# Kernel optimization log

Measured on AMD Instinct MI355X. Metric: run time of the kernel, lower is better.

Reference implementation:

```python
import jax, jax.numpy as jnp
import numpy as np

MARGIN = 0.3
EPS = 1e-12

def setup_inputs() -> dict:
    key = jax.random.key(0)
    k1, k2 = jax.random.split(key)
    n, d, num_classes = 8192, 512, 512
    inputs = jax.random.normal(k1, (n, d), dtype=jnp.float32)
    targets = jax.random.randint(k2, (n,), 0, num_classes, dtype=jnp.int64)
    return {"inputs": inputs, "targets": targets}

def reference(inputs, targets):
    n = inputs.shape[0]
    # pairwise Euclidean distances: ||xi||^2 + ||xj||^2 - 2 xi.xj, clamped & sqrt'd
    sq = jnp.sum(inputs * inputs, axis=1)  # [n]
    dist2 = sq[:, None] + sq[None, :] - 2.0 * (inputs @ inputs.T)
    dist = jnp.sqrt(jnp.clip(dist2, EPS, None))  # [n, n]
    mask = targets[:, None] == targets[None, :]  # [n, n] same-identity mask
    neg_inf = jnp.asarray(-jnp.inf, dist.dtype)
    pos_inf = jnp.asarray(jnp.inf, dist.dtype)
    dist_ap = jnp.max(jnp.where(mask, dist, neg_inf), axis=1)   # hardest positive per row
    dist_an = jnp.min(jnp.where(mask, pos_inf, dist), axis=1)   # hardest negative per row
    # MarginRankingLoss with y=1, mean reduction: mean(relu(dist_ap - dist_an + margin))
    loss = jnp.mean(jnp.maximum(dist_ap - dist_an + MARGIN, 0.0))
    return loss
```

## Files before the change

kernel.cpp:

```cpp
#include <hip/hip_runtime.h>

#define N 8192
#define D 512
#define NSB 32
#define NFULL 1024
#define NQ 64
#define NBRICKS (NFULL + NQ)
#define MARGIN 0.3f

typedef __attribute__((ext_vector_type(4))) int int4v;
typedef __attribute__((ext_vector_type(8))) int int8v;
typedef __attribute__((ext_vector_type(4))) float f32x4;

__device__ __forceinline__ void gload_lds16(const void* g, void* l) {
    __builtin_amdgcn_global_load_lds(
        (const __attribute__((address_space(1))) void*)g,
        (__attribute__((address_space(3))) void*)l,
        16, 0, 0);
}

__device__ __forceinline__ int8v load_frag8(const unsigned char* base, int row, int q) {
    const int v = (2 * q) ^ (row & 7);
    int4v lo = *(const int4v*)(base + row * 128 + v * 16);
    int4v hi = *(const int4v*)(base + row * 128 + (v ^ 1) * 16);
    return __builtin_shufflevector(lo, hi, 0, 1, 2, 3, 4, 5, 6, 7);
}

__global__ void prep_kernel(const float* __restrict__ x,
                            unsigned char* __restrict__ x8,
                            float* __restrict__ sq,
                            unsigned int* __restrict__ apU,
                            unsigned int* __restrict__ anU,
                            int* __restrict__ cnt) {
    if (blockIdx.x == 0 && threadIdx.x == 0) cnt[0] = 0;
    int w = threadIdx.x >> 6, lane = threadIdx.x & 63;
    int row = blockIdx.x * 4 + w;
    const float4* p = (const float4*)(x + (size_t)row * D) + lane * 2;
    float4 v0 = p[0], v1 = p[1];
    float s = v0.x * v0.x + v0.y * v0.y + v0.z * v0.z + v0.w * v0.w
            + v1.x * v1.x + v1.y * v1.y + v1.z * v1.z + v1.w * v1.w;
    int w0 = __builtin_amdgcn_cvt_pk_fp8_f32(v0.x, v0.y, 0, false);
    w0     = __builtin_amdgcn_cvt_pk_fp8_f32(v0.z, v0.w, w0, true);
    int w1 = __builtin_amdgcn_cvt_pk_fp8_f32(v1.x, v1.y, 0, false);
    w1     = __builtin_amdgcn_cvt_pk_fp8_f32(v1.z, v1.w, w1, true);
    ((int2*)(x8 + (size_t)row * D))[lane] = make_int2(w0, w1);
    #pragma unroll
    for (int o = 32; o > 0; o >>= 1) s += __shfl_xor(s, o);
    if (lane == 0) {
        sq[row] = s;
        apU[row] = 0u;
        anU[row] = 0x7f800000u;
    }
}

template <int TN>
__device__ __forceinline__ void brick_body(
    int rowBase, int colBase,
    const unsigned char* __restrict__ xb, const float* __restrict__ sq,
    const int* __restrict__ tgt,
    unsigned int* __restrict__ apU, unsigned int* __restrict__ anU,
    char* smem_raw, float* sqI, float* sqJ, int* tI, int* tJ) {
    constexpr int NC = TN * 32;
    unsigned char* Asm = (unsigned char*)smem_raw;
    unsigned char* Bsm = Asm + 128 * 128;
    float* redAp = (float*)smem_raw;
    float* redAn = redAp + 128 * 34;
    float* colAp = (float*)smem_raw;
    float* colAn = colAp + NC * 10;

    const int tid = threadIdx.x;
    const int w = tid >> 6, lane = tid & 63, q = lane >> 4, c = lane & 15;
    const int wm = w & 1, wn = w >> 1;

    if (tid < 128) { sqI[tid] = sq[rowBase + tid]; tI[tid] = tgt[rowBase + tid]; }
    if (tid < NC)  { sqJ[tid] = sq[colBase + tid]; tJ[tid] = tgt[colBase + tid]; }

    const unsigned char* Ag = xb + (size_t)rowBase * D;
    const unsigned char* Bg = xb + (size_t)colBase * D;

    f32x4 acc[4][TN] = {};

    for (int k0 = 0; k0 < D; k0 += 128) {
        #pragma unroll
        for (int s = 0; s < 4; s++) {
            int p = s * 256 + tid;
            int r = p >> 3, kc = (p & 7) ^ (r & 7);
            gload_lds16(Ag + (size_t)r * D + k0 + kc * 16, Asm + p * 16);
        }
        #pragma unroll
        for (int s = 0; s < TN; s++) {
            int p = s * 256 + tid;
            int r = p >> 3, kc = (p & 7) ^ (r & 7);
            gload_lds16(Bg + (size_t)r * D + k0 + kc * 16, Bsm + p * 16);
        }
        __syncthreads();
        int8v af[4];
        #pragma unroll
        for (int t = 0; t < 4; t++)
            af[t] = load_frag8(Asm, wm * 64 + t * 16 + c, q);
        constexpr int TB = (TN < 4) ? TN : 4;
        #pragma unroll
        for (int tb = 0; tb < TN; tb += TB) {
            int8v bfr[TB];
            #pragma unroll
            for (int t = 0; t < TB; t++)
                bfr[t] = load_frag8(Bsm, wn * (TN * 16) + (tb + t) * 16 + c, q);
            #pragma unroll
            for (int tm = 0; tm < 4; tm++)
                #pragma unroll
                for (int t = 0; t < TB; t++)
                    acc[tm][tb + t] = __builtin_amdgcn_mfma_scale_f32_16x16x128_f8f6f4(
                        af[tm], bfr[t], acc[tm][tb + t],
                        0, 0,
                        0, 0x7F7F7F7Fu, 0, 0x7F7F7F7Fu);
        }
        __syncthreads();
    }

    float sjc[TN]; int tjx[TN];
    #pragma unroll
    for (int tn = 0; tn < TN; tn++) {
        int col_l = wn * (TN * 16) + tn * 16 + c;
        sjc[tn] = sqJ[col_l]; tjx[tn] = tJ[col_l];
    }
    float apc[TN], anc[TN];
    #pragma unroll
    for (int tn = 0; tn < TN; tn++) { apc[tn] = -1e30f; anc[tn] = 1e30f; }
    #pragma unroll
    for (int tm = 0; tm < 4; tm++) {
        #pragma unroll
        for (int r = 0; r < 4; r++) {
            int row_l = wm * 64 + tm * 16 + q * 4 + r;
            float si = sqI[row_l]; int ti = tI[row_l];
            float rp = -1e30f, rn = 1e30f;
            #pragma unroll
            for (int tn = 0; tn < TN; tn++) {
                float p = acc[tm][tn][r];
                bool same = (ti == tjx[tn]);
                float rk = fmaf(-2.0f, p, sjc[tn]);
                float ck = fmaf(-2.0f, p, si);
                rp = fmaxf(rp, same ? rk : -1e30f);
                rn = fminf(rn, same ? 1e30f : rk);
                apc[tn] = fmaxf(apc[tn], same ? ck : -1e30f);
                anc[tn] = fminf(anc[tn], same ? 1e30f : ck);
            }
            redAp[row_l * 34 + wn * 16 + c] = rp;
            redAn[row_l * 34 + wn * 16 + c] = rn;
        }
    }
    __syncthreads();
    if (tid < 128) {
        float ap = -1e30f, an = 1e30f;
        #pragma unroll 8
        for (int u = 0; u < 32; u++) {
            ap = fmaxf(ap, redAp[tid * 34 + u]);
            an = fminf(an, redAn[tid * 34 + u]);
        }
        float apd = fmaxf(sqI[tid] + ap, 0.0f);
        float and_ = fmaxf(sqI[tid] + an, 0.0f);
        atomicMax(&apU[rowBase + tid], __float_as_uint(apd));
        atomicMin(&anU[rowBase + tid], __float_as_uint(and_));
    }
    __syncthreads();
    #pragma unroll
    for (int tn = 0; tn < TN; tn++) {
        int col_l = wn * (TN * 16) + tn * 16 + c;
        colAp[col_l * 10 + wm * 4 + q] = apc[tn];
        colAn[col_l * 10 + wm * 4 + q] = anc[tn];
    }
    __syncthreads();
    if (tid < NC) {
        float ap = -1e30f, an = 1e30f;
        #pragma unroll
        for (int u = 0; u < 8; u++) {
            ap = fmaxf(ap, colAp[tid * 10 + u]);
            an = fminf(an, colAn[tid * 10 + u]);
        }
        float apd = fmaxf(sqJ[tid] + ap, 0.0f);
        float and_ = fmaxf(sqJ[tid] + an, 0.0f);
        atomicMax(&apU[colBase + tid], __float_as_uint(apd));
        atomicMin(&anU[colBase + tid], __float_as_uint(and_));
    }
}

__global__ __launch_bounds__(256, 2)
void gemm_kernel(const unsigned char* __restrict__ xb,
                 const float* __restrict__ sq,
                 const int* __restrict__ tgt,
                 unsigned int* __restrict__ apU,
                 unsigned int* __restrict__ anU) {
    __shared__ __align__(16) char smem_raw[49152];
    __shared__ float sqI[128], sqJ[256];
    __shared__ int tI[128], tJ[256];

    const int id = blockIdx.x;
    if (id < NFULL) {
        int bj2 = (int)sqrtf((float)id + 0.5f);
        while (bj2 * bj2 > id) bj2--;
        while ((bj2 + 1) * (bj2 + 1) <= id) bj2++;
        const int bi = id - bj2 * bj2;
        brick_body<8>(bi * 128, bj2 * 256, xb, sq, tgt, apU, anU,
                      smem_raw, sqI, sqJ, tI, tJ);
    } else {
        const int h = id - NFULL;
        const int j = h >> 1, side = h & 1;
        brick_body<2>((2 * j + 1) * 128, j * 256 + 128 + side * 64,
                      xb, sq, tgt, apU, anU, smem_raw, sqI, sqJ, tI, tJ);
    }
}

__global__ void reduce_kernel(const unsigned int* __restrict__ apU,
                              const unsigned int* __restrict__ anU,
                              float* __restrict__ bsum, int* __restrict__ cnt,
                              float* __restrict__ out) {
    int tid = threadIdx.x;
    int row = blockIdx.x * 256 + tid;
    float ap = __uint_as_float(apU[row]);
    float an = __uint_as_float(anU[row]);
    float dap = sqrtf(fmaxf(ap, 1e-12f));
    float dan = sqrtf(fmaxf(an, 1e-12f));
    float v = fmaxf(dap - dan + MARGIN, 0.0f);
    #pragma unroll
    for (int o = 32; o > 0; o >>= 1) v += __shfl_xor(v, o);
    __shared__ float ss[4];
    __shared__ int amLast;
    if ((tid & 63) == 0) ss[tid >> 6] = v;
    __syncthreads();
    if (tid == 0) {
        bsum[blockIdx.x] = ss[0] + ss[1] + ss[2] + ss[3];
        __threadfence();
        amLast = (atomicAdd(cnt, 1) == N / 256 - 1);
    }
    __syncthreads();
    if (amLast && tid < 64) {
        __threadfence();
        float t = (tid < N / 256) ? bsum[tid] : 0.0f;
        #pragma unroll
        for (int o = 32; o > 0; o >>= 1) t += __shfl_xor(t, o);
        if (tid == 0) out[0] = t * (1.0f / (float)N);
    }
}

extern "C" void kernel_launch(void* const* d_in, const int* in_sizes, int n_in,
                              void* d_out, int out_size, void* d_ws, size_t ws_size,
                              hipStream_t stream) {
    const float* x  = (const float*)d_in[0];
    const int* tgt  = (const int*)d_in[1];
    float* out      = (float*)d_out;

    char* ws = (char*)d_ws;
    unsigned char* x8 = (unsigned char*)ws;
    float* sq   = (float*)(ws + (size_t)N * D);
    unsigned int* apU = (unsigned int*)(sq + N);
    unsigned int* anU = apU + N;
    float* bsum = (float*)(anU + N);
    int* cnt = (int*)(bsum + 32);

    prep_kernel<<<N / 4, 256, 0, stream>>>(x, x8, sq, apU, anU, cnt);
    gemm_kernel<<<NBRICKS, 256, 0, stream>>>(x8, sq, tgt, apU, anU);
    reduce_kernel<<<N / 256, 256, 0, stream>>>(apU, anU, bsum, cnt, out);
}
```

Measured before the change: 104.5 us.

## Load MFMA fragments directly from global memory instead of staging through LDS

Removes the LDS staging of the A and B FP8 tiles (global_load_lds plus swizzled fragment reads) and has each lane read its 32-byte operand fragments straight from global memory. The K loop is fully unrolled and the per-iteration barriers are gone, so the LDS allocation shrinks to what the epilogue reductions need. The aim is to cut LDS traffic and synchronisation and free LDS for occupancy. The cost is that operand reuse across waves now depends on L1/L2 hits, with redundant global loads and less coalesced access.

```diff
diff --git a/kernel.cpp b/kernel.cpp
--- a/kernel.cpp
+++ b/kernel.cpp
@@ -11,20 +11,6 @@
 typedef __attribute__((ext_vector_type(4))) int int4v;
 typedef __attribute__((ext_vector_type(8))) int int8v;
 typedef __attribute__((ext_vector_type(4))) float f32x4;
-
-__device__ __forceinline__ void gload_lds16(const void* g, void* l) {
-    __builtin_amdgcn_global_load_lds(
-        (const __attribute__((address_space(1))) void*)g,
-        (__attribute__((address_space(3))) void*)l,
-        16, 0, 0);
-}
-
-__device__ __forceinline__ int8v load_frag8(const unsigned char* base, int row, int q) {
-    const int v = (2 * q) ^ (row & 7);
-    int4v lo = *(const int4v*)(base + row * 128 + v * 16);
-    int4v hi = *(const int4v*)(base + row * 128 + (v ^ 1) * 16);
-    return __builtin_shufflevector(lo, hi, 0, 1, 2, 3, 4, 5, 6, 7);
-}
 
 __global__ void prep_kernel(const float* __restrict__ x,
                             unsigned char* __restrict__ x8,
@@ -61,8 +47,6 @@
     unsigned int* __restrict__ apU, unsigned int* __restrict__ anU,
     char* smem_raw, float* sqI, float* sqJ, int* tI, int* tJ) {
     constexpr int NC = TN * 32;
-    unsigned char* Asm = (unsigned char*)smem_raw;
-    unsigned char* Bsm = Asm + 128 * 128;
     float* redAp = (float*)smem_raw;
     float* redAn = redAp + 128 * 34;
     float* colAp = (float*)smem_raw;
@@ -75,36 +59,30 @@
     if (tid < 128) { sqI[tid] = sq[rowBase + tid]; tI[tid] = tgt[rowBase + tid]; }
     if (tid < NC)  { sqJ[tid] = sq[colBase + tid]; tJ[tid] = tgt[colBase + tid]; }
 
-    const unsigned char* Ag = xb + (size_t)rowBase * D;
-    const unsigned char* Bg = xb + (size_t)colBase * D;
+    const unsigned char* ap_[4];
+    #pragma unroll
+    for (int t = 0; t < 4; t++)
+        ap_[t] = xb + (size_t)(rowBase + wm * 64 + t * 16 + c) * D + q * 32;
+    const unsigned char* bp_[TN];
+    #pragma unroll
+    for (int t = 0; t < TN; t++)
+        bp_[t] = xb + (size_t)(colBase + wn * (TN * 16) + t * 16 + c) * D + q * 32;
 
     f32x4 acc[4][TN] = {};
 
+    #pragma unroll
     for (int k0 = 0; k0 < D; k0 += 128) {
-        #pragma unroll
-        for (int s = 0; s < 4; s++) {
-            int p = s * 256 + tid;
-            int r = p >> 3, kc = (p & 7) ^ (r & 7);
-            gload_lds16(Ag + (size_t)r * D + k0 + kc * 16, Asm + p * 16);
-        }
-        #pragma unroll
-        for (int s = 0; s < TN; s++) {
-            int p = s * 256 + tid;
-            int r = p >> 3, kc = (p & 7) ^ (r & 7);
-            gload_lds16(Bg + (size_t)r * D + k0 + kc * 16, Bsm + p * 16);
-        }
-        __syncthreads();
         int8v af[4];
         #pragma unroll
         for (int t = 0; t < 4; t++)
-            af[t] = load_frag8(Asm, wm * 64 + t * 16 + c, q);
+            af[t] = *(const int8v*)(ap_[t] + k0);
         constexpr int TB = (TN < 4) ? TN : 4;
         #pragma unroll
         for (int tb = 0; tb < TN; tb += TB) {
             int8v bfr[TB];
             #pragma unroll
             for (int t = 0; t < TB; t++)
-                bfr[t] = load_frag8(Bsm, wn * (TN * 16) + (tb + t) * 16 + c, q);
+                bfr[t] = *(const int8v*)(bp_[tb + t] + k0);
             #pragma unroll
             for (int tm = 0; tm < 4; tm++)
                 #pragma unroll
@@ -114,8 +92,8 @@
                         0, 0,
                         0, 0x7F7F7F7Fu, 0, 0x7F7F7F7Fu);
         }
-        __syncthreads();
-    }
+    }
+    __syncthreads();
 
     float sjc[TN]; int tjx[TN];
     #pragma unroll
@@ -189,7 +167,7 @@
                  const int* __restrict__ tgt,
                  unsigned int* __restrict__ apU,
                  unsigned int* __restrict__ anU) {
-    __shared__ __align__(16) char smem_raw[49152];
+    __shared__ __align__(16) char smem_raw[34816];
     __shared__ float sqI[128], sqJ[256];
     __shared__ int tI[128], tJ[256];
 
```

New measurement: 123.9 us. 1.19x slower.

## Overlap next K-tile global-to-LDS staging with MFMA compute

Applied to the files above, without the earlier changes.

Restructures the K loop so that after fragments are read from LDS into registers, a barrier is taken and the next K-slice's global_load_lds is issued before the remaining MFMAs run. Global load latency should then overlap with matrix compute instead of sitting serialized between barriers. For TN==8 the B fragments are split into two halves so only half the MFMAs wait on the first barrier. The cost is extra live registers, and the single LDS buffer now relies on the barrier ordering to stay correct.

```diff
diff --git a/kernel.cpp b/kernel.cpp
--- a/kernel.cpp
+++ b/kernel.cpp
@@ -24,6 +24,24 @@
     int4v lo = *(const int4v*)(base + row * 128 + v * 16);
     int4v hi = *(const int4v*)(base + row * 128 + (v ^ 1) * 16);
     return __builtin_shufflevector(lo, hi, 0, 1, 2, 3, 4, 5, 6, 7);
+}
+
+template <int TN>
+__device__ __forceinline__ void stage_tiles(const unsigned char* Ag, const unsigned char* Bg,
+                                            unsigned char* Asm, unsigned char* Bsm,
+                                            int tid, int k0) {
+    #pragma unroll
+    for (int s = 0; s < 4; s++) {
+        int p = s * 256 + tid;
+        int r = p >> 3, kc = (p & 7) ^ (r & 7);
+        gload_lds16(Ag + (size_t)r * D + k0 + kc * 16, Asm + p * 16);
+    }
+    #pragma unroll
+    for (int s = 0; s < TN; s++) {
+        int p = s * 256 + tid;
+        int r = p >> 3, kc = (p & 7) ^ (r & 7);
+        gload_lds16(Bg + (size_t)r * D + k0 + kc * 16, Bsm + p * 16);
+    }
 }
 
 __global__ void prep_kernel(const float* __restrict__ x,
@@ -80,41 +98,55 @@
 
     f32x4 acc[4][TN] = {};
 
-    for (int k0 = 0; k0 < D; k0 += 128) {
-        #pragma unroll
-        for (int s = 0; s < 4; s++) {
-            int p = s * 256 + tid;
-            int r = p >> 3, kc = (p & 7) ^ (r & 7);
-            gload_lds16(Ag + (size_t)r * D + k0 + kc * 16, Asm + p * 16);
-        }
-        #pragma unroll
-        for (int s = 0; s < TN; s++) {
-            int p = s * 256 + tid;
-            int r = p >> 3, kc = (p & 7) ^ (r & 7);
-            gload_lds16(Bg + (size_t)r * D + k0 + kc * 16, Bsm + p * 16);
-        }
+    stage_tiles<TN>(Ag, Bg, Asm, Bsm, tid, 0);
+
+    #pragma unroll
+    for (int kk = 0; kk < 4; kk++) {
         __syncthreads();
         int8v af[4];
         #pragma unroll
         for (int t = 0; t < 4; t++)
             af[t] = load_frag8(Asm, wm * 64 + t * 16 + c, q);
         constexpr int TB = (TN < 4) ? TN : 4;
-        #pragma unroll
-        for (int tb = 0; tb < TN; tb += TB) {
-            int8v bfr[TB];
-            #pragma unroll
-            for (int t = 0; t < TB; t++)
-                bfr[t] = load_frag8(Bsm, wn * (TN * 16) + (tb + t) * 16 + c, q);
+        int8v b0[TB];
+        #pragma unroll
+        for (int t = 0; t < TB; t++)
+            b0[t] = load_frag8(Bsm, wn * (TN * 16) + t * 16 + c, q);
+
+        if constexpr (TN == 8) {
+            #pragma unroll
+            for (int tm = 0; tm < 4; tm++)
+                #pragma unroll
+                for (int t = 0; t < 4; t++)
+                    acc[tm][t] = __builtin_amdgcn_mfma_scale_f32_16x16x128_f8f6f4(
+                        af[tm], b0[t], acc[tm][t],
+                        0, 0, 0, 0x7F7F7F7Fu, 0, 0x7F7F7F7Fu);
+            int8v b1[4];
+            #pragma unroll
+            for (int t = 0; t < 4; t++)
+                b1[t] = load_frag8(Bsm, wn * 128 + (4 + t) * 16 + c, q);
+            __syncthreads();
+            if (kk < 3)
+                stage_tiles<8>(Ag, Bg, Asm, Bsm, tid, (kk + 1) * 128);
+            #pragma unroll
+            for (int tm = 0; tm < 4; tm++)
+                #pragma unroll
+                for (int t = 0; t < 4; t++)
+                    acc[tm][4 + t] = __builtin_amdgcn_mfma_scale_f32_16x16x128_f8f6f4(
+                        af[tm], b1[t], acc[tm][4 + t],
+                        0, 0, 0, 0x7F7F7F7Fu, 0, 0x7F7F7F7Fu);
+        } else {
+            __syncthreads();
+            if (kk < 3)
+                stage_tiles<TN>(Ag, Bg, Asm, Bsm, tid, (kk + 1) * 128);
             #pragma unroll
             for (int tm = 0; tm < 4; tm++)
                 #pragma unroll
                 for (int t = 0; t < TB; t++)
-                    acc[tm][tb + t] = __builtin_amdgcn_mfma_scale_f32_16x16x128_f8f6f4(
-                        af[tm], bfr[t], acc[tm][tb + t],
-                        0, 0,
-                        0, 0x7F7F7F7Fu, 0, 0x7F7F7F7Fu);
-        }
-        __syncthreads();
+                    acc[tm][t] = __builtin_amdgcn_mfma_scale_f32_16x16x128_f8f6f4(
+                        af[tm], b0[t], acc[tm][t],
+                        0, 0, 0, 0x7F7F7F7Fu, 0, 0x7F7F7F7Fu);
+        }
     }
 
     float sjc[TN]; int tjx[TN];
```

Measured after the change: 98.93 us. 1.06x faster.

## Double-buffer LDS tiles with explicit vmcnt waits and 512-thread blocks

Applied to the files above, without the earlier changes.

The GEMM brick kernel now runs 8 waves per block instead of 4, with each wave owning a narrower column slice. The K-loop is unrolled and uses two LDS buffers, so global-to-LDS loads for step k+2 are issued while the MFMAs for step k run. Fine-grained s_waitcnt vmcnt/lgkmcnt plus raw barriers replace the full __syncthreads, and s_setprio raises priority during the MFMA phase. Doubling LDS to 96KB per block likely allows only one block per CU, and the row reduction now has to scan 64 partials per row.

```diff
diff --git a/kernel.cpp b/kernel.cpp
--- a/kernel.cpp
+++ b/kernel.cpp
@@ -2,7 +2,6 @@
 
 #define N 8192
 #define D 512
-#define NSB 32
 #define NFULL 1024
 #define NQ 64
 #define NBRICKS (NFULL + NQ)
@@ -24,6 +23,24 @@
     int4v lo = *(const int4v*)(base + row * 128 + v * 16);
     int4v hi = *(const int4v*)(base + row * 128 + (v ^ 1) * 16);
     return __builtin_shufflevector(lo, hi, 0, 1, 2, 3, 4, 5, 6, 7);
+}
+
+template <int TNW>
+__device__ __forceinline__ void stage_tiles(const unsigned char* Ag, const unsigned char* Bg,
+                                            unsigned char* Asm, unsigned char* Bsm,
+                                            int tid, int k0) {
+    #pragma unroll
+    for (int s = 0; s < 2; s++) {
+        int p = s * 512 + tid;
+        int r = p >> 3, kc = (p & 7) ^ (r & 7);
+        gload_lds16(Ag + (size_t)r * D + k0 + kc * 16, Asm + p * 16);
+    }
+    #pragma unroll
+    for (int s = 0; s < TNW; s++) {
+        int p = s * 512 + tid;
+        int r = p >> 3, kc = (p & 7) ^ (r & 7);
+        gload_lds16(Bg + (size_t)r * D + k0 + kc * 16, Bsm + p * 16);
+    }
 }
 
 __global__ void prep_kernel(const float* __restrict__ x,
@@ -53,18 +70,21 @@
     }
 }
 
-template <int TN>
+template <int TNW>
 __device__ __forceinline__ void brick_body(
     int rowBase, int colBase,
     const unsigned char* __restrict__ xb, const float* __restrict__ sq,
     const int* __restrict__ tgt,
     unsigned int* __restrict__ apU, unsigned int* __restrict__ anU,
     char* smem_raw, float* sqI, float* sqJ, int* tI, int* tJ) {
-    constexpr int NC = TN * 32;
-    unsigned char* Asm = (unsigned char*)smem_raw;
-    unsigned char* Bsm = Asm + 128 * 128;
+    constexpr int NC = 64 * TNW;
+    constexpr int S = 16384 + NC * 128;
+    unsigned char* A0 = (unsigned char*)smem_raw;
+    unsigned char* B0 = A0 + 16384;
+    unsigned char* A1 = A0 + S;
+    unsigned char* B1 = A1 + 16384;
     float* redAp = (float*)smem_raw;
-    float* redAn = redAp + 128 * 34;
+    float* redAn = redAp + 128 * 66;
     float* colAp = (float*)smem_raw;
     float* colAn = colAp + NC * 10;
 
@@ -78,54 +98,61 @@
     const unsigned char* Ag = xb + (size_t)rowBase * D;
     const unsigned char* Bg = xb + (size_t)colBase * D;
 
-    f32x4 acc[4][TN] = {};
-
-    for (int k0 = 0; k0 < D; k0 += 128) {
-        #pragma unroll
-        for (int s = 0; s < 4; s++) {
-            int p = s * 256 + tid;
-            int r = p >> 3, kc = (p & 7) ^ (r & 7);
-            gload_lds16(Ag + (size_t)r * D + k0 + kc * 16, Asm + p * 16);
-        }
-        #pragma unroll
-        for (int s = 0; s < TN; s++) {
-            int p = s * 256 + tid;
-            int r = p >> 3, kc = (p & 7) ^ (r & 7);
-            gload_lds16(Bg + (size_t)r * D + k0 + kc * 16, Bsm + p * 16);
-        }
-        __syncthreads();
+    f32x4 acc[4][TNW] = {};
+
+    stage_tiles<TNW>(Ag, Bg, A0, B0, tid, 0);
+    stage_tiles<TNW>(Ag, Bg, A1, B1, tid, 128);
+
+    #pragma unroll
+    for (int kk = 0; kk < 4; kk++) {
+        unsigned char* Asm = (kk & 1) ? A1 : A0;
+        unsigned char* Bsm = (kk & 1) ? B1 : B0;
+        if (kk < 3) {
+            if constexpr (TNW == 4) asm volatile("s_waitcnt vmcnt(6)" ::: "memory");
+            else                    asm volatile("s_waitcnt vmcnt(3)" ::: "memory");
+        } else {
+            asm volatile("s_waitcnt vmcnt(0)" ::: "memory");
+        }
+        __builtin_amdgcn_s_barrier();
+        __builtin_amdgcn_sched_barrier(0);
+
         int8v af[4];
         #pragma unroll
         for (int t = 0; t < 4; t++)
             af[t] = load_frag8(Asm, wm * 64 + t * 16 + c, q);
-        constexpr int TB = (TN < 4) ? TN : 4;
-        #pragma unroll
-        for (int tb = 0; tb < TN; tb += TB) {
-            int8v bfr[TB];
+        int8v bf[TNW];
+        #pragma unroll
+        for (int t = 0; t < TNW; t++)
+            bf[t] = load_frag8(Bsm, wn * (TNW * 16) + t * 16 + c, q);
+
+        asm volatile("s_waitcnt lgkmcnt(0)" ::: "memory");
+        __builtin_amdgcn_s_barrier();
+        __builtin_amdgcn_sched_barrier(0);
+
+        if (kk < 2)
+            stage_tiles<TNW>(Ag, Bg, Asm, Bsm, tid, (kk + 2) * 128);
+
+        __builtin_amdgcn_s_setprio(1);
+        #pragma unroll
+        for (int tm = 0; tm < 4; tm++)
             #pragma unroll
-            for (int t = 0; t < TB; t++)
-                bfr[t] = load_frag8(Bsm, wn * (TN * 16) + (tb + t) * 16 + c, q);
-            #pragma unroll
-            for (int tm = 0; tm < 4; tm++)
-                #pragma unroll
-                for (int t = 0; t < TB; t++)
-                    acc[tm][tb + t] = __builtin_amdgcn_mfma_scale_f32_16x16x128_f8f6f4(
-                        af[tm], bfr[t], acc[tm][tb + t],
-                        0, 0,
-                        0, 0x7F7F7F7Fu, 0, 0x7F7F7F7Fu);
-        }
-        __syncthreads();
-    }
-
-    float sjc[TN]; int tjx[TN];
-    #pragma unroll
-    for (int tn = 0; tn < TN; tn++) {
-        int col_l = wn * (TN * 16) + tn * 16 + c;
+            for (int t = 0; t < TNW; t++)
+                acc[tm][t] = __builtin_amdgcn_mfma_scale_f32_16x16x128_f8f6f4(
+                    af[tm], bf[t], acc[tm][t],
+                    0, 0,
+                    0, 0x7F7F7F7Fu, 0, 0x7F7F7F7Fu);
+        __builtin_amdgcn_s_setprio(0);
+    }
+
+    float sjc[TNW]; int tjx[TNW];
+    #pragma unroll
+    for (int tn = 0; tn < TNW; tn++) {
+        int col_l = wn * (TNW * 16) + tn * 16 + c;
         sjc[tn] = sqJ[col_l]; tjx[tn] = tJ[col_l];
     }
-    float apc[TN], anc[TN];
-    #pragma unroll
-    for (int tn = 0; tn < TN; tn++) { apc[tn] = -1e30f; anc[tn] = 1e30f; }
+    float apc[TNW], anc[TNW];
+    #pragma unroll
+    for (int tn = 0; tn < TNW; tn++) { apc[tn] = -1e30f; anc[tn] = 1e30f; }
     #pragma unroll
     for (int tm = 0; tm < 4; tm++) {
         #pragma unroll
@@ -134,7 +161,7 @@
             float si = sqI[row_l]; int ti = tI[row_l];
             float rp = -1e30f, rn = 1e30f;
             #pragma unroll
-            for (int tn = 0; tn < TN; tn++) {
+            for (int tn = 0; tn < TNW; tn++) {
                 float p = acc[tm][tn][r];
                 bool same = (ti == tjx[tn]);
                 float rk = fmaf(-2.0f, p, sjc[tn]);
@@ -144,17 +171,17 @@
                 apc[tn] = fmaxf(apc[tn], same ? ck : -1e30f);
                 anc[tn] = fminf(anc[tn], same ? 1e30f : ck);
             }
-            redAp[row_l * 34 + wn * 16 + c] = rp;
-            redAn[row_l * 34 + wn * 16 + c] = rn;
+            redAp[row_l * 66 + wn * 16 + c] = rp;
+            redAn[row_l * 66 + wn * 16 + c] = rn;
         }
     }
     __syncthreads();
     if (tid < 128) {
         float ap = -1e30f, an = 1e30f;
         #pragma unroll 8
-        for (int u = 0; u < 32; u++) {
-            ap = fmaxf(ap, redAp[tid * 34 + u]);
-            an = fminf(an, redAn[tid * 34 + u]);
+        for (int u = 0; u < 64; u++) {
+            ap = fmaxf(ap, redAp[tid * 66 + u]);
+            an = fminf(an, redAn[tid * 66 + u]);
         }
         float apd = fmaxf(sqI[tid] + ap, 0.0f);
         float and_ = fmaxf(sqI[tid] + an, 0.0f);
@@ -163,8 +190,8 @@
     }
     __syncthreads();
     #pragma unroll
-    for (int tn = 0; tn < TN; tn++) {
-        int col_l = wn * (TN * 16) + tn * 16 + c;
+    for (int tn = 0; tn < TNW; tn++) {
+        int col_l = wn * (TNW * 16) + tn * 16 + c;
         colAp[col_l * 10 + wm * 4 + q] = apc[tn];
         colAn[col_l * 10 + wm * 4 + q] = anc[tn];
     }
@@ -183,13 +210,13 @@
     }
 }
 
-__global__ __launch_bounds__(256, 2)
+__global__ __launch_bounds__(512, 2)
 void gemm_kernel(const unsigned char* __restrict__ xb,
                  const float* __restrict__ sq,
                  const int* __restrict__ tgt,
                  unsigned int* __restrict__ apU,
                  unsigned int* __restrict__ anU) {
-    __shared__ __align__(16) char smem_raw[49152];
+    __shared__ __align__(16) char smem_raw[98304];
     __shared__ float sqI[128], sqJ[256];
     __shared__ int tI[128], tJ[256];
 
@@ -199,12 +226,12 @@
         while (bj2 * bj2 > id) bj2--;
         while ((bj2 + 1) * (bj2 + 1) <= id) bj2++;
         const int bi = id - bj2 * bj2;
-        brick_body<8>(bi * 128, bj2 * 256, xb, sq, tgt, apU, anU,
+        brick_body<4>(bi * 128, bj2 * 256, xb, sq, tgt, apU, anU,
                       smem_raw, sqI, sqJ, tI, tJ);
     } else {
         const int h = id - NFULL;
         const int j = h >> 1, side = h & 1;
-        brick_body<2>((2 * j + 1) * 128, j * 256 + 128 + side * 64,
+        brick_body<1>((2 * j + 1) * 128, j * 256 + 128 + side * 64,
                       xb, sq, tgt, apU, anU, smem_raw, sqI, sqJ, tI, tJ);
     }
 }
@@ -257,6 +284,6 @@
     int* cnt = (int*)(bsum + 32);
 
     prep_kernel<<<N / 4, 256, 0, stream>>>(x, x8, sq, apU, anU, cnt);
-    gemm_kernel<<<NBRICKS, 256, 0, stream>>>(x8, sq, tgt, apU, anU);
+    gemm_kernel<<<NBRICKS, 512, 0, stream>>>(x8, sq, tgt, apU, anU);
     reduce_kernel<<<N / 256, 256, 0, stream>>>(apU, anU, bsum, cnt, out);
 }
```

New measurement: 110.5 us. 5.7% more time.
